# Optimization experiments

Hardware: AMD Instinct MI355X
Metric: run time of the kernel (lower is better)

Reference implementation:

```python
import jax, jax.numpy as jnp
import numpy as np

DIM = 1024
NUM_HEADS = 16
DIM_PROJ = int(2 / 3 * 4 * DIM // 8 * 8)  # 2728, per source
EPS = 1e-5


def rms_norm(x, g):
    # NOTE: source computes sqrt(mean(x^2)) then divides by (rms + eps)
    rms = jnp.sqrt(jnp.mean(x * x, axis=-1, keepdims=True))
    return x / (rms + EPS) * g


def alibi_slopes(num_heads):
    base = (2.0 ** 8) ** (1.0 / num_heads)
    return jnp.asarray([1.0 / base ** (i + 1) for i in range(num_heads)], dtype=jnp.float32)


def setup_inputs() -> dict:
    key = jax.random.key(0)
    ks = jax.random.split(key, 7)
    B, T, C, P = 2, 2048, DIM, DIM_PROJ
    s = 0.02
    return {
        "x": jax.random.normal(ks[0], (B, T, C), dtype=jnp.float32),
        "g1": jnp.ones((C,), dtype=jnp.float32),
        "w_qkv": jax.random.normal(ks[1], (C, 3 * C), dtype=jnp.float32) * s,
        "w_o": jax.random.normal(ks[2], (C, C), dtype=jnp.float32) * s,
        "g2": jnp.ones((C,), dtype=jnp.float32),
        "W": jax.random.normal(ks[3], (C, P), dtype=jnp.float32) * s,
        "V": jax.random.normal(ks[4], (C, P), dtype=jnp.float32) * s,
        "W2": jax.random.normal(ks[5], (P, C), dtype=jnp.float32) * s,
    }


def reference(x, g1, w_qkv, w_o, g2, W, V, W2):
    B, T, C = x.shape
    H = NUM_HEADS
    Dh = C // H

    # --- attention sublayer ---
    h = rms_norm(x, g1)
    qkv = h @ w_qkv                              # [B,T,3C]
    q, k, v = jnp.split(qkv, 3, axis=-1)
    q = q.reshape(B, T, H, Dh).transpose(0, 2, 1, 3)  # [B,H,T,Dh]
    k = k.reshape(B, T, H, Dh).transpose(0, 2, 1, 3)
    v = v.reshape(B, T, H, Dh).transpose(0, 2, 1, 3)

    wei = jnp.einsum('bhqd,bhkd->bhqk', q, k)
    pos = jnp.arange(T)
    rel = (pos[None, :] - pos[:, None]).astype(jnp.float32)  # [T,T]
    m = alibi_slopes(H)[:, None, None]                        # [H,1,1]
    scale = C ** 0.5                                          # sqrt(dim), per source
    scores = wei / scale + m * rel
    causal = pos[None, :] <= pos[:, None]                     # [T,T]
    scores = jnp.where(causal[None, None], scores, -jnp.inf)
    attn = jax.nn.softmax(scores, axis=-1)

    out = jnp.einsum('bhqk,bhkd->bhqd', attn, v)
    concat = out.transpose(0, 2, 1, 3).reshape(B, T, C)
    x = concat @ w_o + x

    # --- SwiGLU sublayer ---
    h = rms_norm(x, g2)
    gated = jax.nn.silu(h @ W) * (h @ V)
    return gated @ W2 + x
```

## Files before the change

### kernel.cpp

```cpp
#include <hip/hip_runtime.h>
#include <math.h>

typedef __attribute__((ext_vector_type(8))) short bf16x8;
typedef __attribute__((ext_vector_type(4))) float f32x4;

static __device__ __forceinline__ short f2bf(float x){
  union { float f; unsigned u; } a; a.f = x;
  unsigned r = a.u + 0x7fffu + ((a.u >> 16) & 1u);
  return (short)(r >> 16);
}

__global__ __launch_bounds__(256) void transpose_bf16_kernel(
    const float* __restrict__ in, short* __restrict__ out,
    int IR, int IC, int OR, int OC)
{
  __shared__ float tile[32][33];
  int i0 = blockIdx.x * 32;
  int j0 = blockIdx.y * 32;
  int tx = threadIdx.x, ty = threadIdx.y;
  #pragma unroll
  for (int r = 0; r < 32; r += 8){
    int j = j0 + ty + r, i = i0 + tx;
    tile[ty + r][tx] = (j < IR && i < IC) ? in[(size_t)j * IC + i] : 0.f;
  }
  __syncthreads();
  #pragma unroll
  for (int r = 0; r < 32; r += 8){
    int oi = i0 + ty + r, oj = j0 + tx;
    if (oi < OR && oj < OC) out[(size_t)oi * OC + oj] = f2bf(tile[tx][ty + r]);
  }
}

__global__ __launch_bounds__(256) void transpose_bb_kernel(
    const short* __restrict__ in, short* __restrict__ out)
{
  __shared__ short tile[32][33];
  int bh = blockIdx.z;
  int t0 = blockIdx.x * 32;
  int d0 = blockIdx.y * 32;
  int tx = threadIdx.x, ty = threadIdx.y;
  const short* src = in + ((size_t)bh * 2048 + t0) * 64 + d0;
  #pragma unroll
  for (int r = 0; r < 32; r += 8)
    tile[ty + r][tx] = src[(size_t)(ty + r) * 64 + tx];
  __syncthreads();
  short* dst = out + ((size_t)bh * 64 + d0) * 2048 + t0;
  #pragma unroll
  for (int r = 0; r < 32; r += 8)
    dst[(size_t)(ty + r) * 2048 + tx] = tile[tx][ty + r];
}

__global__ __launch_bounds__(256) void rmsnorm_kernel(
    const float* __restrict__ x, const float* __restrict__ g, short* __restrict__ out)
{
  int row = blockIdx.x, tid = threadIdx.x;
  const float4* xr = (const float4*)(x + (size_t)row * 1024);
  float4 v = xr[tid];
  float ss = v.x*v.x + v.y*v.y + v.z*v.z + v.w*v.w;
  #pragma unroll
  for (int m = 1; m < 64; m <<= 1) ss += __shfl_xor(ss, m, 64);
  __shared__ float sm[4];
  if ((tid & 63) == 0) sm[tid >> 6] = ss;
  __syncthreads();
  float tot = sm[0] + sm[1] + sm[2] + sm[3];
  float inv = 1.f / (sqrtf(tot * (1.f/1024.f)) + 1e-5f);
  float4 gv = ((const float4*)g)[tid];
  short4 o;
  o.x = f2bf(v.x * inv * gv.x);
  o.y = f2bf(v.y * inv * gv.y);
  o.z = f2bf(v.z * inv * gv.z);
  o.w = f2bf(v.w * inv * gv.w);
  *(short4*)(out + (size_t)row * 1024 + tid * 4) = o;
}

enum { EPI_F32 = 0, EPI_RESID = 1, EPI_QKV = 2, EPI_GATED = 3 };


template<int BM, int BN>
static __device__ __forceinline__ void dp_issue(
    const short* __restrict__ A, const short* __restrict__ Bt,
    short* __restrict__ lbuf, int K, int m0, int n0, int k0,
    int wave, int lane, int l)
{
  int g = (l * 8 + wave) * 64 + lane;
  const short* src;
  if (g < BM * 8){
    int row = g >> 3, cc = g & 7;
    src = A + (size_t)(m0 + row) * K + k0 + ((cc ^ (row & 7)) << 3);
  } else {
    int gb = g - BM * 8;
    int row = gb >> 3, cc = gb & 7;
    src = Bt + (size_t)(n0 + row) * K + k0 + ((cc ^ (row & 7)) << 3);
  }
  __builtin_amdgcn_global_load_lds((const __attribute__((address_space(1))) void*)src,
                                   (__attribute__((address_space(3))) void*)(lbuf + (size_t)g * 8),
                                   16, 0, 0);
}

template<int BM, int BN, int EPI>
__global__ __launch_bounds__(512, 2) void gemm_dp_kernel(
    const short* __restrict__ A, const short* __restrict__ Bt,
    int M, int N, int K,
    float* __restrict__ outF, short* __restrict__ outB,
    const float* __restrict__ resid, const float* __restrict__ Gprev,
    short* __restrict__ qb, short* __restrict__ kb, short* __restrict__ vb)
{
  constexpr int L  = (BM + BN) / 64;
  constexpr int WM = BM / 2, WN = BN / 4;
  constexpr int FR = WM / 16, FC = WN / 16;
  __shared__ short lds[2][(BM + BN) * 64];
  const int tid = threadIdx.x, lane = tid & 63, wave = tid >> 6;
  const int wr = wave >> 2, wc = wave & 3;
  const int la = lane & 15, lg = lane >> 4;

  int nbn = N / BN;
  int nwg = (M / BM) * nbn;
  int bid = blockIdx.x;
  int wg = ((nwg & 7) == 0) ? ((bid & 7) * (nwg >> 3) + (bid >> 3)) : bid;
  int m0 = (wg / nbn) * BM, n0 = (wg % nbn) * BN;

  f32x4 acc[FR][FC];
  #pragma unroll
  for (int i = 0; i < FR; ++i)
    #pragma unroll
    for (int j = 0; j < FC; ++j) acc[i][j] = f32x4{0.f, 0.f, 0.f, 0.f};

  const int NT = K >> 6;

  #pragma unroll
  for (int l = 0; l < L; ++l) dp_issue<BM, BN>(A, Bt, lds[0], K, m0, n0, 0,  wave, lane, l);
  #pragma unroll
  for (int l = 0; l < L; ++l) dp_issue<BM, BN>(A, Bt, lds[1], K, m0, n0, 64, wave, lane, l);

  for (int t = 0; t < NT; ++t){
    short* curb = lds[t & 1];
    if (t + 1 < NT){
      if constexpr (L == 8) asm volatile("s_waitcnt vmcnt(8)" ::: "memory");
      else                  asm volatile("s_waitcnt vmcnt(4)" ::: "memory");
    } else {
      asm volatile("s_waitcnt vmcnt(0)" ::: "memory");
    }
    __builtin_amdgcn_s_barrier();
    __builtin_amdgcn_sched_barrier(0);

    #pragma unroll
    for (int qr = 0; qr < FR / 4; ++qr){
      #pragma unroll
      for (int qc = 0; qc < FC / 2; ++qc){
        bf16x8 af[4][2], bfv[2][2];
        #pragma unroll
        for (int ii = 0; ii < 4; ++ii){
          int r = wr * WM + (qr * 4 + ii) * 16 + la;
          #pragma unroll
          for (int ks = 0; ks < 2; ++ks)
            af[ii][ks] = *(const bf16x8*)(curb + r * 64 + (((ks * 4 + lg) ^ (r & 7)) << 3));
        }
        #pragma unroll
        for (int jc = 0; jc < 2; ++jc){
          int rb = wc * WN + (qc * 2 + jc) * 16 + la;
          #pragma unroll
          for (int ks = 0; ks < 2; ++ks)
            bfv[jc][ks] = *(const bf16x8*)(curb + BM * 64 + rb * 64 + (((ks * 4 + lg) ^ (rb & 7)) << 3));
        }
        __builtin_amdgcn_s_setprio(1);
        #pragma unroll
        for (int ii = 0; ii < 4; ++ii)
          #pragma unroll
          for (int jc = 0; jc < 2; ++jc){
            acc[qr*4+ii][qc*2+jc] = __builtin_amdgcn_mfma_f32_16x16x32_bf16(
                af[ii][0], bfv[jc][0], acc[qr*4+ii][qc*2+jc], 0, 0, 0);
            acc[qr*4+ii][qc*2+jc] = __builtin_amdgcn_mfma_f32_16x16x32_bf16(
                af[ii][1], bfv[jc][1], acc[qr*4+ii][qc*2+jc], 0, 0, 0);
          }
        __builtin_amdgcn_s_setprio(0);
      }
    }
    __builtin_amdgcn_sched_barrier(0);
    __builtin_amdgcn_s_barrier();
    __builtin_amdgcn_sched_barrier(0);
    if (t + 2 < NT){
      #pragma unroll
      for (int l = 0; l < L; ++l)
        dp_issue<BM, BN>(A, Bt, curb, K, m0, n0, (t + 2) << 6, wave, lane, l);
    }
  }

  #pragma unroll
  for (int i = 0; i < FR; ++i){
    #pragma unroll
    for (int j = 0; j < FC; ++j){
      #pragma unroll
      for (int rr = 0; rr < 4; ++rr){
        int row = m0 + wr * WM + i * 16 + lg * 4 + rr;
        int col = n0 + wc * WN + j * 16 + la;
        float v = acc[i][j][rr];
        size_t idx = (size_t)row * N + col;
        if (EPI == EPI_F32){
          outF[idx] = v;
        } else if (EPI == EPI_RESID){
          outF[idx] = v + resid[idx];
        } else if (EPI == EPI_GATED){
          float gg = Gprev[idx];
          float s = gg / (1.f + __expf(-gg));
          outB[idx] = f2bf(s * v);
        } else {
          int which = col >> 10;
          int hh = (col & 1023) >> 6;
          int d = col & 63;
          int bb = row >> 11, tt = row & 2047;
          size_t o = (((size_t)(bb * 16 + hh) * 2048) + tt) * 64 + d;
          if (which == 0)      qb[o] = f2bf(v * 0.03125f);
          else if (which == 1) kb[o] = f2bf(v);
          else                 vb[o] = f2bf(v);
        }
      }
    }
  }
}

__global__ __launch_bounds__(512) void attn_kernel(
    const short* __restrict__ qb, const short* __restrict__ kb,
    const short* __restrict__ vtb, short* __restrict__ concat)
{
  const int T = 2048;
  int bh = blockIdx.y;
  int h = bh & 15, b = bh >> 4;
  int p = blockIdx.x;
  int tid = threadIdx.x, lane = tid & 63, wave = tid >> 6;
  int la = lane & 15, lg = lane >> 4;

  const short* Q  = qb  + (size_t)bh * T * 64;
  const short* Kg = kb  + (size_t)bh * T * 64;
  const short* Vt = vtb + (size_t)bh * 64 * T;

  __shared__ short Ks[2][64][72];
  __shared__ short Vs[2][64][72];
  __shared__ short Ps[8][16][72];

  int srow = tid >> 3, scol = (tid & 7) * 8;
  float slope = exp2f(-0.5f * (float)(h + 1));

  for (int half = 0; half < 2; ++half){
    int j = half ? (15 - p) : p;
    int ntiles = 2 * j + 2;

    int qr = j * 128 + wave * 16 + la;
    bf16x8 qf0 = *(const bf16x8*)(Q + (size_t)qr * 64 + lg * 8);
    bf16x8 qf1 = *(const bf16x8*)(Q + (size_t)qr * 64 + 32 + lg * 8);

    f32x4 o[4];
    float m_run[4], l_run[4];
    #pragma unroll
    for (int i = 0; i < 4; ++i){ o[i] = f32x4{0.f,0.f,0.f,0.f}; m_run[i] = -1e30f; l_run[i] = 0.f; }

    {
      bf16x8 k0 = *(const bf16x8*)(Kg + (size_t)srow * 64 + scol);
      bf16x8 v0 = *(const bf16x8*)(Vt + (size_t)srow * T + scol);
      *(bf16x8*)&Ks[0][srow][scol] = k0;
      *(bf16x8*)&Vs[0][srow][scol] = v0;
    }
    __syncthreads();

    int qpb = j * 128 + wave * 16 + lg * 4;

    for (int t = 0; t < ntiles; ++t){
      int cur = t & 1;
      int kv0 = t * 64;
      bool pref = (t + 1 < ntiles);
      bf16x8 kreg, vreg;
      if (pref){
        kreg = *(const bf16x8*)(Kg + (size_t)((t + 1) * 64 + srow) * 64 + scol);
        vreg = *(const bf16x8*)(Vt + (size_t)srow * T + (t + 1) * 64 + scol);
      }

      f32x4 s[4];
      #pragma unroll
      for (int nt = 0; nt < 4; ++nt){
        f32x4 a0 = f32x4{0.f,0.f,0.f,0.f};
        a0 = __builtin_amdgcn_mfma_f32_16x16x32_bf16(qf0, *(const bf16x8*)&Ks[cur][nt*16+la][lg*8],    a0, 0, 0, 0);
        a0 = __builtin_amdgcn_mfma_f32_16x16x32_bf16(qf1, *(const bf16x8*)&Ks[cur][nt*16+la][32+lg*8], a0, 0, 0, 0);
        s[nt] = a0;
      }

      float pbuf[4][4];
      #pragma unroll
      for (int r = 0; r < 4; ++r){
        int qpos = qpb + r;
        float mx = -1e30f;
        #pragma unroll
        for (int nt = 0; nt < 4; ++nt){
          int kvpos = kv0 + nt * 16 + la;
          float sc = s[nt][r] + slope * (float)(kvpos - qpos);
          sc = (kvpos <= qpos) ? sc : -1e30f;
          pbuf[nt][r] = sc;
          mx = fmaxf(mx, sc);
        }
        mx = fmaxf(mx, __shfl_xor(mx, 1, 16));
        mx = fmaxf(mx, __shfl_xor(mx, 2, 16));
        mx = fmaxf(mx, __shfl_xor(mx, 4, 16));
        mx = fmaxf(mx, __shfl_xor(mx, 8, 16));
        float mnew = fmaxf(m_run[r], mx);
        float alpha = __expf(m_run[r] - mnew);
        m_run[r] = mnew;
        float ps = 0.f;
        #pragma unroll
        for (int nt = 0; nt < 4; ++nt){
          float pe = __expf(pbuf[nt][r] - mnew);
          pbuf[nt][r] = pe;
          ps += pe;
        }
        ps += __shfl_xor(ps, 1, 16);
        ps += __shfl_xor(ps, 2, 16);
        ps += __shfl_xor(ps, 4, 16);
        ps += __shfl_xor(ps, 8, 16);
        l_run[r] = l_run[r] * alpha + ps;
        #pragma unroll
        for (int dt = 0; dt < 4; ++dt) o[dt][r] *= alpha;
      }

      #pragma unroll
      for (int r = 0; r < 4; ++r)
        #pragma unroll
        for (int nt = 0; nt < 4; ++nt)
          Ps[wave][lg * 4 + r][nt * 16 + la] = f2bf(pbuf[nt][r]);

      #pragma unroll
      for (int ks = 0; ks < 2; ++ks){
        bf16x8 pa = *(const bf16x8*)&Ps[wave][la][ks * 32 + lg * 8];
        #pragma unroll
        for (int dt = 0; dt < 4; ++dt){
          bf16x8 bv = *(const bf16x8*)&Vs[cur][dt * 16 + la][ks * 32 + lg * 8];
          o[dt] = __builtin_amdgcn_mfma_f32_16x16x32_bf16(pa, bv, o[dt], 0, 0, 0);
        }
      }

      if (pref){
        *(bf16x8*)&Ks[cur ^ 1][srow][scol] = kreg;
        *(bf16x8*)&Vs[cur ^ 1][srow][scol] = vreg;
      }
      __syncthreads();
    }

    #pragma unroll
    for (int dt = 0; dt < 4; ++dt){
      #pragma unroll
      for (int r = 0; r < 4; ++r){
        int qpos = qpb + r;
        int d = dt * 16 + la;
        float val = o[dt][r] / l_run[r];
        concat[((size_t)(b * 2048 + qpos)) * 1024 + h * 64 + d] = f2bf(val);
      }
    }
  }
}

extern "C" void kernel_launch(void* const* d_in, const int* in_sizes, int n_in,
                              void* d_out, int out_size, void* d_ws, size_t ws_size,
                              hipStream_t stream)
{
  (void)in_sizes; (void)n_in; (void)out_size; (void)ws_size;
  const float* x     = (const float*)d_in[0];
  const float* g1    = (const float*)d_in[1];
  const float* w_qkv = (const float*)d_in[2];
  const float* w_o   = (const float*)d_in[3];
  const float* g2    = (const float*)d_in[4];
  const float* W     = (const float*)d_in[5];
  const float* V     = (const float*)d_in[6];
  const float* W2    = (const float*)d_in[7];
  float* out = (float*)d_out;

  char* wsb = (char*)d_ws;
  size_t off = 0;
  auto alloc = [&](size_t bytes) -> void* {
    void* p = wsb + off;
    off += (bytes + 255) & ~(size_t)255;
    return p;
  };
  short* wqkvT = (short*)alloc((size_t)3072 * 1024 * 2);
  short* woT   = (short*)alloc((size_t)1024 * 1024 * 2);
  short* WT    = (short*)alloc((size_t)2816 * 1024 * 2);
  short* VT    = (short*)alloc((size_t)2816 * 1024 * 2);
  short* W2T   = (short*)alloc((size_t)1024 * 2816 * 2);
  short* h1    = (short*)alloc((size_t)4096 * 1024 * 2);
  short* qbuf  = (short*)alloc((size_t)4096 * 1024 * 2);
  short* kbuf  = (short*)alloc((size_t)4096 * 1024 * 2);
  short* vbuf  = (short*)alloc((size_t)4096 * 1024 * 2);
  short* vtbuf = (short*)alloc((size_t)4096 * 1024 * 2);
  short* conc  = (short*)alloc((size_t)4096 * 1024 * 2);
  float* x2    = (float*)alloc((size_t)4096 * 1024 * 4);
  short* h2    = (short*)alloc((size_t)4096 * 1024 * 2);
  float* G     = (float*)alloc((size_t)4096 * 2816 * 4);
  short* gated = (short*)alloc((size_t)4096 * 2816 * 2);

  dim3 tb(32, 8);
  hipLaunchKernelGGL(transpose_bf16_kernel, dim3(96, 32), tb, 0, stream, w_qkv, wqkvT, 1024, 3072, 3072, 1024);
  hipLaunchKernelGGL(transpose_bf16_kernel, dim3(32, 32), tb, 0, stream, w_o,   woT,   1024, 1024, 1024, 1024);
  hipLaunchKernelGGL(transpose_bf16_kernel, dim3(88, 32), tb, 0, stream, W,     WT,    1024, 2728, 2816, 1024);
  hipLaunchKernelGGL(transpose_bf16_kernel, dim3(88, 32), tb, 0, stream, V,     VT,    1024, 2728, 2816, 1024);
  hipLaunchKernelGGL(transpose_bf16_kernel, dim3(32, 88), tb, 0, stream, W2,    W2T,   2728, 1024, 1024, 2816);

  hipLaunchKernelGGL(rmsnorm_kernel, dim3(4096), dim3(256), 0, stream, x, g1, h1);

  hipLaunchKernelGGL((gemm_dp_kernel<256, 256, EPI_QKV>), dim3(192), dim3(512), 0, stream,
                     h1, wqkvT, 4096, 3072, 1024,
                     (float*)nullptr, (short*)nullptr, (const float*)nullptr, (const float*)nullptr,
                     qbuf, kbuf, vbuf);

  hipLaunchKernelGGL(transpose_bb_kernel, dim3(64, 2, 32), tb, 0, stream, vbuf, vtbuf);

  hipLaunchKernelGGL(attn_kernel, dim3(8, 32), dim3(512), 0, stream, qbuf, kbuf, vtbuf, conc);

  hipLaunchKernelGGL((gemm_dp_kernel<128, 128, EPI_RESID>), dim3(256), dim3(512), 0, stream,
                     conc, woT, 4096, 1024, 1024,
                     x2, (short*)nullptr, x, (const float*)nullptr,
                     (short*)nullptr, (short*)nullptr, (short*)nullptr);

  hipLaunchKernelGGL(rmsnorm_kernel, dim3(4096), dim3(256), 0, stream, x2, g2, h2);

  hipLaunchKernelGGL((gemm_dp_kernel<256, 256, EPI_F32>), dim3(176), dim3(512), 0, stream,
                     h2, WT, 4096, 2816, 1024,
                     G, (short*)nullptr, (const float*)nullptr, (const float*)nullptr,
                     (short*)nullptr, (short*)nullptr, (short*)nullptr);

  hipLaunchKernelGGL((gemm_dp_kernel<256, 256, EPI_GATED>), dim3(176), dim3(512), 0, stream,
                     h2, VT, 4096, 2816, 1024,
                     (float*)nullptr, gated, (const float*)nullptr, G,
                     (short*)nullptr, (short*)nullptr, (short*)nullptr);

  hipLaunchKernelGGL((gemm_dp_kernel<128, 128, EPI_RESID>), dim3(256), dim3(512), 0, stream,
                     gated, W2T, 4096, 1024, 2816,
                     out, (short*)nullptr, x2, (const float*)nullptr,
                     (short*)nullptr, (short*)nullptr, (short*)nullptr);
}
```

Measured before the change: 299.4 us.

## Restructure attention into many small blocks reading K/V directly from global memory

The attention kernel goes from 256 blocks of 512 threads, each pairing two 128-row query tiles to balance causal work, to 1024 blocks of 256 threads, each owning one 64-row query tile. Blocks are ordered so the longest tiles launch first and neighbouring blocks share a head. The shared-memory double buffering of K and V tiles, and the block barriers that came with it, are removed, so each wave loads its K and V MFMA fragments straight from global memory and relies on the caches for reuse. This gives more blocks and occupancy with no barriers, at the cost of redundant global/L2 traffic, since each of the 4 waves now re-reads the same K/V tile and the loads are no longer prefetched ahead of use.

```diff
diff --git a/kernel.cpp b/kernel.cpp
--- a/kernel.cpp
+++ b/kernel.cpp
@@ -74,7 +74,6 @@
 }
 
 enum { EPI_F32 = 0, EPI_RESID = 1, EPI_QKV = 2, EPI_GATED = 3 };
-
 
 template<int BM, int BN>
 static __device__ __forceinline__ void dp_issue(
@@ -218,14 +217,16 @@
   }
 }
 
-__global__ __launch_bounds__(512) void attn_kernel(
+__global__ __launch_bounds__(256) void attn_kernel(
     const short* __restrict__ qb, const short* __restrict__ kb,
     const short* __restrict__ vtb, short* __restrict__ concat)
 {
   const int T = 2048;
-  int bh = blockIdx.y;
+  int id = blockIdx.x;
+  int rr = id & 7, sidx = id >> 3;
+  int bh = rr + 8 * (sidx & 3);
+  int j  = 31 - (sidx >> 2);
   int h = bh & 15, b = bh >> 4;
-  int p = blockIdx.x;
   int tid = threadIdx.x, lane = tid & 63, wave = tid >> 6;
   int la = lane & 15, lg = lane >> 4;
 
@@ -233,123 +234,98 @@
   const short* Kg = kb  + (size_t)bh * T * 64;
   const short* Vt = vtb + (size_t)bh * 64 * T;
 
-  __shared__ short Ks[2][64][72];
-  __shared__ short Vs[2][64][72];
-  __shared__ short Ps[8][16][72];
-
-  int srow = tid >> 3, scol = (tid & 7) * 8;
+  __shared__ short Ps[4][16][72];
+
   float slope = exp2f(-0.5f * (float)(h + 1));
 
-  for (int half = 0; half < 2; ++half){
-    int j = half ? (15 - p) : p;
-    int ntiles = 2 * j + 2;
-
-    int qr = j * 128 + wave * 16 + la;
-    bf16x8 qf0 = *(const bf16x8*)(Q + (size_t)qr * 64 + lg * 8);
-    bf16x8 qf1 = *(const bf16x8*)(Q + (size_t)qr * 64 + 32 + lg * 8);
-
-    f32x4 o[4];
-    float m_run[4], l_run[4];
-    #pragma unroll
-    for (int i = 0; i < 4; ++i){ o[i] = f32x4{0.f,0.f,0.f,0.f}; m_run[i] = -1e30f; l_run[i] = 0.f; }
-
-    {
-      bf16x8 k0 = *(const bf16x8*)(Kg + (size_t)srow * 64 + scol);
-      bf16x8 v0 = *(const bf16x8*)(Vt + (size_t)srow * T + scol);
-      *(bf16x8*)&Ks[0][srow][scol] = k0;
-      *(bf16x8*)&Vs[0][srow][scol] = v0;
-    }
-    __syncthreads();
-
-    int qpb = j * 128 + wave * 16 + lg * 4;
-
-    for (int t = 0; t < ntiles; ++t){
-      int cur = t & 1;
-      int kv0 = t * 64;
-      bool pref = (t + 1 < ntiles);
-      bf16x8 kreg, vreg;
-      if (pref){
-        kreg = *(const bf16x8*)(Kg + (size_t)((t + 1) * 64 + srow) * 64 + scol);
-        vreg = *(const bf16x8*)(Vt + (size_t)srow * T + (t + 1) * 64 + scol);
+  int qr = j * 64 + wave * 16 + la;
+  bf16x8 qf0 = *(const bf16x8*)(Q + (size_t)qr * 64 + lg * 8);
+  bf16x8 qf1 = *(const bf16x8*)(Q + (size_t)qr * 64 + 32 + lg * 8);
+
+  f32x4 o[4];
+  float m_run[4], l_run[4];
+  #pragma unroll
+  for (int i = 0; i < 4; ++i){ o[i] = f32x4{0.f,0.f,0.f,0.f}; m_run[i] = -1e30f; l_run[i] = 0.f; }
+
+  int qpb = j * 64 + wave * 16 + lg * 4;
+  int ntiles = j + 1;
+
+  for (int t = 0; t < ntiles; ++t){
+    int kv0 = t * 64;
+    const short* Kt = Kg + (size_t)kv0 * 64;
+
+    f32x4 s4[4];
+    #pragma unroll
+    for (int nt = 0; nt < 4; ++nt){
+      bf16x8 kf0 = *(const bf16x8*)(Kt + (size_t)(nt * 16 + la) * 64 + lg * 8);
+      bf16x8 kf1 = *(const bf16x8*)(Kt + (size_t)(nt * 16 + la) * 64 + 32 + lg * 8);
+      f32x4 a0 = f32x4{0.f,0.f,0.f,0.f};
+      a0 = __builtin_amdgcn_mfma_f32_16x16x32_bf16(qf0, kf0, a0, 0, 0, 0);
+      a0 = __builtin_amdgcn_mfma_f32_16x16x32_bf16(qf1, kf1, a0, 0, 0, 0);
+      s4[nt] = a0;
+    }
+
+    float pbuf[4][4];
+    #pragma unroll
+    for (int r = 0; r < 4; ++r){
+      int qpos = qpb + r;
+      float mx = -1e30f;
+      #pragma unroll
+      for (int nt = 0; nt < 4; ++nt){
+        int kvpos = kv0 + nt * 16 + la;
+        float sc = s4[nt][r] + slope * (float)(kvpos - qpos);
+        sc = (kvpos <= qpos) ? sc : -1e30f;
+        pbuf[nt][r] = sc;
+        mx = fmaxf(mx, sc);
       }
-
-      f32x4 s[4];
+      mx = fmaxf(mx, __shfl_xor(mx, 1, 16));
+      mx = fmaxf(mx, __shfl_xor(mx, 2, 16));
+      mx = fmaxf(mx, __shfl_xor(mx, 4, 16));
+      mx = fmaxf(mx, __shfl_xor(mx, 8, 16));
+      float mnew = fmaxf(m_run[r], mx);
+      float alpha = __expf(m_run[r] - mnew);
+      m_run[r] = mnew;
+      float ps = 0.f;
       #pragma unroll
       for (int nt = 0; nt < 4; ++nt){
-        f32x4 a0 = f32x4{0.f,0.f,0.f,0.f};
-        a0 = __builtin_amdgcn_mfma_f32_16x16x32_bf16(qf0, *(const bf16x8*)&Ks[cur][nt*16+la][lg*8],    a0, 0, 0, 0);
-        a0 = __builtin_amdgcn_mfma_f32_16x16x32_bf16(qf1, *(const bf16x8*)&Ks[cur][nt*16+la][32+lg*8], a0, 0, 0, 0);
-        s[nt] = a0;
+        float pe = __expf(pbuf[nt][r] - mnew);
+        pbuf[nt][r] = pe;
+        ps += pe;
       }
-
-      float pbuf[4][4];
-      #pragma unroll
-      for (int r = 0; r < 4; ++r){
-        int qpos = qpb + r;
-        float mx = -1e30f;
-        #pragma unroll
-        for (int nt = 0; nt < 4; ++nt){
-          int kvpos = kv0 + nt * 16 + la;
-          float sc = s[nt][r] + slope * (float)(kvpos - qpos);
-          sc = (kvpos <= qpos) ? sc : -1e30f;
-          pbuf[nt][r] = sc;
-          mx = fmaxf(mx, sc);
-        }
-        mx = fmaxf(mx, __shfl_xor(mx, 1, 16));
-        mx = fmaxf(mx, __shfl_xor(mx, 2, 16));
-        mx = fmaxf(mx, __shfl_xor(mx, 4, 16));
-        mx = fmaxf(mx, __shfl_xor(mx, 8, 16));
-        float mnew = fmaxf(m_run[r], mx);
-        float alpha = __expf(m_run[r] - mnew);
-        m_run[r] = mnew;
-        float ps = 0.f;
-        #pragma unroll
-        for (int nt = 0; nt < 4; ++nt){
-          float pe = __expf(pbuf[nt][r] - mnew);
-          pbuf[nt][r] = pe;
-          ps += pe;
-        }
-        ps += __shfl_xor(ps, 1, 16);
-        ps += __shfl_xor(ps, 2, 16);
-        ps += __shfl_xor(ps, 4, 16);
-        ps += __shfl_xor(ps, 8, 16);
-        l_run[r] = l_run[r] * alpha + ps;
-        #pragma unroll
-        for (int dt = 0; dt < 4; ++dt) o[dt][r] *= alpha;
+      ps += __shfl_xor(ps, 1, 16);
+      ps += __shfl_xor(ps, 2, 16);
+      ps += __shfl_xor(ps, 4, 16);
+      ps += __shfl_xor(ps, 8, 16);
+      l_run[r] = l_run[r] * alpha + ps;
+      #pragma unroll
+      for (int dt = 0; dt < 4; ++dt) o[dt][r] *= alpha;
+    }
+
+    #pragma unroll
+    for (int r = 0; r < 4; ++r)
+      #pragma unroll
+      for (int nt = 0; nt < 4; ++nt)
+        Ps[wave][lg * 4 + r][nt * 16 + la] = f2bf(pbuf[nt][r]);
+
+    #pragma unroll
+    for (int ks = 0; ks < 2; ++ks){
+      bf16x8 pa = *(const bf16x8*)&Ps[wave][la][ks * 32 + lg * 8];
+      #pragma unroll
+      for (int dt = 0; dt < 4; ++dt){
+        bf16x8 bv = *(const bf16x8*)(Vt + (size_t)(dt * 16 + la) * T + kv0 + ks * 32 + lg * 8);
+        o[dt] = __builtin_amdgcn_mfma_f32_16x16x32_bf16(pa, bv, o[dt], 0, 0, 0);
       }
-
-      #pragma unroll
-      for (int r = 0; r < 4; ++r)
-        #pragma unroll
-        for (int nt = 0; nt < 4; ++nt)
-          Ps[wave][lg * 4 + r][nt * 16 + la] = f2bf(pbuf[nt][r]);
-
-      #pragma unroll
-      for (int ks = 0; ks < 2; ++ks){
-        bf16x8 pa = *(const bf16x8*)&Ps[wave][la][ks * 32 + lg * 8];
-        #pragma unroll
-        for (int dt = 0; dt < 4; ++dt){
-          bf16x8 bv = *(const bf16x8*)&Vs[cur][dt * 16 + la][ks * 32 + lg * 8];
-          o[dt] = __builtin_amdgcn_mfma_f32_16x16x32_bf16(pa, bv, o[dt], 0, 0, 0);
-        }
-      }
-
-      if (pref){
-        *(bf16x8*)&Ks[cur ^ 1][srow][scol] = kreg;
-        *(bf16x8*)&Vs[cur ^ 1][srow][scol] = vreg;
-      }
-      __syncthreads();
-    }
-
-    #pragma unroll
-    for (int dt = 0; dt < 4; ++dt){
-      #pragma unroll
-      for (int r = 0; r < 4; ++r){
-        int qpos = qpb + r;
-        int d = dt * 16 + la;
-        float val = o[dt][r] / l_run[r];
-        concat[((size_t)(b * 2048 + qpos)) * 1024 + h * 64 + d] = f2bf(val);
-      }
+    }
+  }
+
+  #pragma unroll
+  for (int dt = 0; dt < 4; ++dt){
+    #pragma unroll
+    for (int r = 0; r < 4; ++r){
+      int qpos = qpb + r;
+      int d = dt * 16 + la;
+      float val = o[dt][r] / l_run[r];
+      concat[((size_t)(b * 2048 + qpos)) * 1024 + h * 64 + d] = f2bf(val);
     }
   }
 }
@@ -408,7 +384,7 @@
 
   hipLaunchKernelGGL(transpose_bb_kernel, dim3(64, 2, 32), tb, 0, stream, vbuf, vtbuf);
 
-  hipLaunchKernelGGL(attn_kernel, dim3(8, 32), dim3(512), 0, stream, qbuf, kbuf, vtbuf, conc);
+  hipLaunchKernelGGL(attn_kernel, dim3(1024), dim3(256), 0, stream, qbuf, kbuf, vtbuf, conc);
 
   hipLaunchKernelGGL((gemm_dp_kernel<128, 128, EPI_RESID>), dim3(256), dim3(512), 0, stream,
                      conc, woT, 4096, 1024, 1024,
```

Result: slower. 365.9 us (+22.2%).
